# Performance work log

Measured on AMD Instinct MI355X. Metric: run time of the kernel, lower is better.

The kernel has to match this reference:

```python
import math
import jax, jax.numpy as jnp
import numpy as np

D_MODEL = 256
N_HEADS = 4
HEAD_DIM = D_MODEL // N_HEADS
MAX_REL = 30


def _rel_pos_encodings(t, d_model):
    # sinusoidal table over clipped relative distances -> [t, t, d_model]
    n = 2 * MAX_REL + 1
    positions = jnp.arange(n, dtype=jnp.float32)[:, None]
    div_term = jnp.exp(jnp.arange(0, d_model, 2, dtype=jnp.float32) * (-math.log(10000.0) / d_model))
    ang = positions * div_term                      # [n, d/2]
    enc = jnp.stack([jnp.sin(ang), jnp.cos(ang)], axis=-1).reshape(n, d_model)
    rng = jnp.arange(t)
    final_mat = jnp.clip(rng[None, :] - rng[:, None], -MAX_REL, MAX_REL) + MAX_REL  # [t, t]
    return enc[final_mat]                           # [t, t, d_model]


def setup_inputs() -> dict:
    key = jax.random.key(0)
    ks = jax.random.split(key, 12)
    d = D_MODEL
    s = 1.0 / math.sqrt(d)
    inp = {
        "inputs": jax.random.normal(ks[0], (16, 512, d), dtype=jnp.float32),
        "ln_gamma": jnp.ones((d,), jnp.float32),
        "ln_beta": jnp.zeros((d,), jnp.float32),
        "Wq": jax.random.normal(ks[1], (d, d), jnp.float32) * s,
        "bq": jnp.zeros((d,), jnp.float32),
        "Wk": jax.random.normal(ks[2], (d, d), jnp.float32) * s,
        "bk": jnp.zeros((d,), jnp.float32),
        "Wv": jax.random.normal(ks[3], (d, d), jnp.float32) * s,
        "bv": jnp.zeros((d,), jnp.float32),
        "Wpos": jax.random.normal(ks[4], (d, d), jnp.float32) * s,
        "bpos": jnp.zeros((d,), jnp.float32),
        "Wo": jax.random.normal(ks[5], (d, d), jnp.float32) * s,
        "bo": jnp.zeros((d,), jnp.float32),
        "u_bias": jax.random.normal(ks[6], (1, N_HEADS, 1, HEAD_DIM), jnp.float32) * 0.02,
        "v_bias": jax.random.normal(ks[7], (1, N_HEADS, 1, HEAD_DIM), jnp.float32) * 0.02,
    }
    return inp


def reference(inputs, ln_gamma, ln_beta, Wq, bq, Wk, bk, Wv, bv, Wpos, bpos, Wo, bo, u_bias, v_bias):
    b, t, d = inputs.shape
    h, hd = N_HEADS, HEAD_DIM
    # LayerNorm (eps=1e-5, torch default)
    mu = jnp.mean(inputs, axis=-1, keepdims=True)
    var = jnp.mean(jnp.square(inputs - mu), axis=-1, keepdims=True)
    x = (inputs - mu) * jax.lax.rsqrt(var + 1e-5) * ln_gamma + ln_beta

    def split_heads(y):
        return y.reshape(b, t, h, hd).transpose(0, 2, 1, 3)  # b h t d

    q = split_heads(x @ Wq.T + bq)
    k = split_heads(x @ Wk.T + bk)
    v = split_heads(x @ Wv.T + bv)

    rel = jax.lax.stop_gradient(_rel_pos_encodings(t, d))    # [t, t, d]
    pos = (rel @ Wpos.T + bpos).reshape(t, t, h, hd)         # [t1, t2, h, hd]

    qk_score = jnp.einsum('bhtd,bhsd->bhts', q + u_bias, k)
    pos_score = jnp.einsum('bhtd,tshd->bhts', q + v_bias, pos)
    scores = (qk_score + pos_score) / math.sqrt(hd)
    attn = jax.nn.softmax(scores, axis=-1)
    ctx = jnp.einsum('bhts,bhsd->bhtd', attn, v)
    ctx = ctx.transpose(0, 2, 1, 3).reshape(b, t, d)
    return ctx @ Wo.T + bo
```

## Files before the change

kernel.cpp:

```cpp
#include <hip/hip_runtime.h>
#include <hip/hip_bf16.h>
#include <math.h>

#define B 16
#define T 512
#define D 256
#define H 4
#define HD 64
#define MAXREL 30
#define NREL 61
#define M_ROWS (B*T)
#define QBLK 128

typedef __attribute__((ext_vector_type(8))) short bf16x8;
typedef __attribute__((ext_vector_type(4))) float f32x4;
typedef unsigned short ush;

__device__ inline ush f2b(float f) {
    __hip_bfloat16 h = __float2bfloat16(f);
    union { __hip_bfloat16 h; ush u; } c; c.h = h; return c.u;
}
__device__ inline float b2f(ush u) {
    union { ush u; __hip_bfloat16 h; } c; c.u = u; return __bfloat162float(c.h);
}
__device__ inline unsigned int pk2(float a, float b) {
    __hip_bfloat162 h = __float22bfloat162_rn(make_float2(a, b));
    union { __hip_bfloat162 h; unsigned int u; } c; c.h = h; return c.u;
}
__device__ inline int swz(int row, int byteoff) {
    return row * 128 + (byteoff ^ ((row & 7) << 4));
}
__device__ inline int swz256(int row, int byteoff) {
    return row * 256 + (byteoff ^ ((row & 7) << 4));
}
__device__ inline int swz512(int row, int byteoff) {
    return row * 512 + (byteoff ^ ((row & 7) << 4));
}

#define SCL 0.1803368801111204f

__global__ __launch_bounds__(256) void prep_kernel(const float* __restrict__ x,
                                                   const float* __restrict__ gamma,
                                                   const float* __restrict__ beta,
                                                   ush* __restrict__ xb,
                                                   const float* __restrict__ Wq, const float* __restrict__ Wk,
                                                   const float* __restrict__ Wv, const float* __restrict__ Wo,
                                                   ush* __restrict__ wb,
                                                   const float* __restrict__ Wpos,
                                                   const float* __restrict__ bpos,
                                                   ush* __restrict__ pospb) {
    __shared__ __attribute__((aligned(16))) ush wpS[64 * 256];
    int bid = blockIdx.x;
    int tid = threadIdx.x;
    if (bid < 512) {
        int lane = tid & 63;
        float4 g = *(const float4*)(gamma + lane * 4);
        float4 bb = *(const float4*)(beta + lane * 4);
        #pragma unroll
        for (int it = 0; it < 4; ++it) {
            int row = bid * 16 + it * 4 + (tid >> 6);
            const float* xr = x + (size_t)row * D;
            float4 v = *(const float4*)(xr + lane * 4);
            float s = v.x + v.y + v.z + v.w;
            #pragma unroll
            for (int off = 32; off; off >>= 1) s += __shfl_xor(s, off);
            float mu = s * (1.f / 256.f);
            float dx = v.x - mu, dy = v.y - mu, dz = v.z - mu, dw = v.w - mu;
            float vs = dx*dx + dy*dy + dz*dz + dw*dw;
            #pragma unroll
            for (int off = 32; off; off >>= 1) vs += __shfl_xor(vs, off);
            float rstd = rsqrtf(vs * (1.f / 256.f) + 1e-5f);
            ushort4 o;
            o.x = f2b(dx * rstd * g.x + bb.x);
            o.y = f2b(dy * rstd * g.y + bb.y);
            o.z = f2b(dz * rstd * g.z + bb.z);
            o.w = f2b(dw * rstd * g.w + bb.w);
            *(ushort4*)(xb + (size_t)row * D + lane * 4) = o;
        }
    } else if (bid < 512 + 256) {
        int b2 = bid - 512;
        int z = b2 >> 6, xblk = b2 & 63;
        const float* src = z == 0 ? Wq : z == 1 ? Wk : z == 2 ? Wv : Wo;
        int idx = (xblk * 256 + tid) * 4;
        float4 v = *(const float4*)(src + idx);
        ushort4 o;
        o.x = f2b(v.x); o.y = f2b(v.y); o.z = f2b(v.z); o.w = f2b(v.w);
        *(ushort4*)(wb + (size_t)z * 65536 + idx) = o;
    } else {
        int h = bid - 768;
        int w = tid >> 6, l = tid & 63, lg = l >> 4, ln = l & 15;
        const float* wsrc = Wpos + (size_t)(h * 64) * D;
        #pragma unroll
        for (int c = 0; c < 16; ++c) {
            int idx = c * 256 + tid;
            int row = idx >> 6, col = (idx & 63) * 4;
            float4 v = *(const float4*)(wsrc + (size_t)row * D + col);
            ushort4 o; o.x = f2b(v.x); o.y = f2b(v.y); o.z = f2b(v.z); o.w = f2b(v.w);
            *(ushort4*)((char*)wpS + swz512(row, col * 2)) = o;
        }
        int p = w * 16 + ln;
        bf16x8 af[8];
        #pragma unroll
        for (int ks = 0; ks < 8; ++ks) {
            #pragma unroll
            for (int j = 0; j < 8; ++j) {
                int k = ks * 32 + lg * 8 + j;
                int i = k >> 1;
                float dt = __expf(-(2.f * i) * (9.210340371976184f / 256.f));
                float ang = (float)p * dt;
                float v = (k & 1) ? __cosf(ang) : __sinf(ang);
                af[ks][j] = (short)f2b(v);
            }
        }
        __syncthreads();
        f32x4 acc[4] = {};
        #pragma unroll
        for (int ks = 0; ks < 8; ++ks) {
            int kbyte = (ks * 32 + lg * 8) * 2;
            #pragma unroll
            for (int ct = 0; ct < 4; ++ct) {
                bf16x8 bf = *(const bf16x8*)((const char*)wpS + swz512(ct * 16 + ln, kbyte));
                acc[ct] = __builtin_amdgcn_mfma_f32_16x16x32_bf16(af[ks], bf, acc[ct], 0, 0, 0);
            }
        }
        #pragma unroll
        for (int ct = 0; ct < 4; ++ct) {
            int dcol = ct * 16 + ln;
            float bb = bpos[h * 64 + dcol];
            #pragma unroll
            for (int r = 0; r < 4; ++r) {
                int pr = w * 16 + lg * 4 + r;
                pospb[(size_t)h * 4096 + pr * 64 + dcol] = f2b(acc[ct][r] + bb);
            }
        }
    }
}

__global__ __launch_bounds__(256, 3) void qkv_mfma(const ush* __restrict__ A,
                                                   const ush* __restrict__ wball,
                                                   const float* __restrict__ bq,
                                                   const float* __restrict__ bk,
                                                   const float* __restrict__ bv,
                                                   ush* __restrict__ qb,
                                                   ush* __restrict__ kbuf,
                                                   ush* __restrict__ vtb) {
    __shared__ __attribute__((aligned(16))) ush A_s[128 * 128];
    __shared__ __attribute__((aligned(16))) ush B_s[64 * 128];
    int tid = threadIdx.x;
    int w = tid >> 6, l = tid & 63;
    int lg = l >> 4, ln = l & 15;
    int wr = w >> 1, wc = w & 1;
    int i0 = blockIdx.x * 128;
    int j0 = blockIdx.y * 64;
    int z = blockIdx.z;
    const ush* Wp = wball + (size_t)z * 65536 + (size_t)j0 * D;
    const ush* Ap = A + (size_t)i0 * D;
    const float* bias = z == 0 ? bq : (z == 1 ? bk : bv);
    f32x4 acc[2][4] = {};

    #pragma unroll 1
    for (int kb2 = 0; kb2 < 2; ++kb2) {
        int k0 = kb2 * 128;
        if (kb2) __syncthreads();
        #pragma unroll
        for (int c = 0; c < 8; ++c) {
            int u = c * 256 + tid;
            int row = u >> 4, sub = u & 15;
            *(bf16x8*)((char*)A_s + swz256(row, sub * 16)) = *(const bf16x8*)(Ap + (size_t)row * D + k0 + sub * 8);
        }
        #pragma unroll
        for (int c = 0; c < 4; ++c) {
            int u = c * 256 + tid;
            int row = u >> 4, sub = u & 15;
            *(bf16x8*)((char*)B_s + swz256(row, sub * 16)) = *(const bf16x8*)(Wp + (size_t)row * D + k0 + sub * 8);
        }
        __syncthreads();
        __builtin_amdgcn_s_setprio(1);
        #pragma unroll
        for (int ksub = 0; ksub < 4; ++ksub) {
            int kbyte = ksub * 64 + lg * 16;
            bf16x8 af[2], bfr[4];
            #pragma unroll
            for (int mi = 0; mi < 2; ++mi)
                af[mi] = *(const bf16x8*)((const char*)B_s + swz256(wr * 32 + mi * 16 + ln, kbyte));
            #pragma unroll
            for (int ni = 0; ni < 4; ++ni)
                bfr[ni] = *(const bf16x8*)((const char*)A_s + swz256(wc * 64 + ni * 16 + ln, kbyte));
            #pragma unroll
            for (int mi = 0; mi < 2; ++mi)
                #pragma unroll
                for (int ni = 0; ni < 4; ++ni)
                    acc[mi][ni] = __builtin_amdgcn_mfma_f32_16x16x32_bf16(af[mi], bfr[ni], acc[mi][ni], 0, 0, 0);
        }
        __builtin_amdgcn_s_setprio(0);
    }

    if (z == 2) {
        #pragma unroll
        for (int mi = 0; mi < 2; ++mi) {
            int jb = j0 + wr * 32 + mi * 16 + lg * 4;
            float4 bv4 = *(const float4*)(bias + jb);
            float bvv[4] = {bv4.x, bv4.y, bv4.z, bv4.w};
            #pragma unroll
            for (int ni = 0; ni < 4; ++ni) {
                int t = i0 + wc * 64 + ni * 16 + ln;
                #pragma unroll
                for (int r = 0; r < 4; ++r)
                    vtb[(size_t)(jb + r) * M_ROWS + t] = f2b(acc[mi][ni][r] + bvv[r]);
            }
        }
    } else {
        ush* ob = (z == 0) ? qb : kbuf;
        #pragma unroll
        for (int mi = 0; mi < 2; ++mi) {
            int jb = j0 + wr * 32 + mi * 16 + lg * 4;
            float4 bv4 = *(const float4*)(bias + jb);
            #pragma unroll
            for (int ni = 0; ni < 4; ++ni) {
                int t = i0 + wc * 64 + ni * 16 + ln;
                ushort4 o;
                o.x = f2b(acc[mi][ni][0] + bv4.x); o.y = f2b(acc[mi][ni][1] + bv4.y);
                o.z = f2b(acc[mi][ni][2] + bv4.z); o.w = f2b(acc[mi][ni][3] + bv4.w);
                *(ushort4*)(ob + (size_t)t * D + jb) = o;
            }
        }
    }
}

__global__ __launch_bounds__(256, 2) void outproj_mfma(const ush* __restrict__ A,
                                                       const ush* __restrict__ W,
                                                       const float* __restrict__ bias,
                                                       float* __restrict__ of) {
    __shared__ __attribute__((aligned(16))) ush A_s[64 * 128];
    __shared__ __attribute__((aligned(16))) ush B_s[64 * 128];
    int tid = threadIdx.x;
    int w = tid >> 6, l = tid & 63;
    int lg = l >> 4, ln = l & 15;
    int wr = w >> 1, wc = w & 1;
    int i0 = blockIdx.x * 64;
    int j0 = blockIdx.y * 64;
    const ush* Ap = A + (size_t)i0 * D;
    const ush* Wp = W + (size_t)j0 * D;
    f32x4 acc[2][2] = {};

    #pragma unroll 1
    for (int kb2 = 0; kb2 < 2; ++kb2) {
        int k0 = kb2 * 128;
        if (kb2) __syncthreads();
        #pragma unroll
        for (int c = 0; c < 4; ++c) {
            int u = c * 256 + tid;
            int row = u >> 4, sub = u & 15;
            *(bf16x8*)((char*)A_s + swz256(row, sub * 16)) = *(const bf16x8*)(Ap + (size_t)row * D + k0 + sub * 8);
            *(bf16x8*)((char*)B_s + swz256(row, sub * 16)) = *(const bf16x8*)(Wp + (size_t)row * D + k0 + sub * 8);
        }
        __syncthreads();
        __builtin_amdgcn_s_setprio(1);
        #pragma unroll
        for (int ksub = 0; ksub < 4; ++ksub) {
            int kbyte = ksub * 64 + lg * 16;
            bf16x8 af[2], bfr[2];
            #pragma unroll
            for (int mi = 0; mi < 2; ++mi)
                af[mi] = *(const bf16x8*)((const char*)B_s + swz256(wr * 32 + mi * 16 + ln, kbyte));
            #pragma unroll
            for (int ni = 0; ni < 2; ++ni)
                bfr[ni] = *(const bf16x8*)((const char*)A_s + swz256(wc * 32 + ni * 16 + ln, kbyte));
            #pragma unroll
            for (int mi = 0; mi < 2; ++mi)
                #pragma unroll
                for (int ni = 0; ni < 2; ++ni)
                    acc[mi][ni] = __builtin_amdgcn_mfma_f32_16x16x32_bf16(af[mi], bfr[ni], acc[mi][ni], 0, 0, 0);
        }
        __builtin_amdgcn_s_setprio(0);
    }

    #pragma unroll
    for (int mi = 0; mi < 2; ++mi) {
        int jb = j0 + wr * 32 + mi * 16 + lg * 4;
        float4 bv4 = *(const float4*)(bias + jb);
        #pragma unroll
        for (int ni = 0; ni < 2; ++ni) {
            int t = i0 + wc * 32 + ni * 16 + ln;
            float4 o;
            o.x = acc[mi][ni][0] + bv4.x; o.y = acc[mi][ni][1] + bv4.y;
            o.z = acc[mi][ni][2] + bv4.z; o.w = acc[mi][ni][3] + bv4.w;
            *(float4*)(of + (size_t)t * D + jb) = o;
        }
    }
}

__global__ __launch_bounds__(512, 2) void attn_mfma(const ush* __restrict__ qb,
                                                    const ush* __restrict__ kb,
                                                    const ush* __restrict__ vtb,
                                                    const ush* __restrict__ pospb,
                                                    const float* __restrict__ u_bias,
                                                    const float* __restrict__ v_bias,
                                                    ush* __restrict__ ctxb) {
    __shared__ __attribute__((aligned(16))) ush Kd[2][64 * 64];
    __shared__ __attribute__((aligned(16))) ush Vd[2][64 * 64];
    __shared__ __attribute__((aligned(16))) ush pdS[8][16 * 66];
    __shared__ __attribute__((aligned(16))) ush PlS[8][16 * 64];

    int tid = threadIdx.x;
    int w = tid >> 6;
    int l = tid & 63;
    int lg = l >> 4, ln = l & 15;
    int bh = blockIdx.x;
    int b = bh >> 2, h = bh & 3;
    int t0 = blockIdx.y * QBLK;
    const size_t baseBH = ((size_t)b * T) * D + h * HD;

    bf16x8 qu[2], qv[2];
    {
        const ush* qrow = qb + baseBH + (size_t)(t0 + w * 16 + ln) * D;
        int c0 = lg * 8;
        #pragma unroll
        for (int ks = 0; ks < 2; ++ks) {
            bf16x8 ld = *(const bf16x8*)(qrow + ks * 32 + c0);
            float4 ub0 = *(const float4*)(u_bias + h * HD + ks * 32 + c0);
            float4 ub1 = *(const float4*)(u_bias + h * HD + ks * 32 + c0 + 4);
            float4 vb0 = *(const float4*)(v_bias + h * HD + ks * 32 + c0);
            float4 vb1 = *(const float4*)(v_bias + h * HD + ks * 32 + c0 + 4);
            float ubv[8] = {ub0.x,ub0.y,ub0.z,ub0.w,ub1.x,ub1.y,ub1.z,ub1.w};
            float vbv[8] = {vb0.x,vb0.y,vb0.z,vb0.w,vb1.x,vb1.y,vb1.z,vb1.w};
            #pragma unroll
            for (int j = 0; j < 8; ++j) {
                float f = b2f((ush)ld[j]);
                qu[ks][j] = (short)f2b((f + ubv[j]) * SCL);
                qv[ks][j] = (short)f2b((f + vbv[j]) * SCL);
            }
        }
    }

    int r0 = tid >> 3, c0 = tid & 7;
    const ush* kbase = kb + baseBH;
    const ush* vbase = vtb + (size_t)(h * HD) * M_ROWS + (size_t)b * T;
    const ush* pbase = pospb + (size_t)h * 4096;

    {
        bf16x8 pp0 = *(const bf16x8*)(pbase + r0 * 64 + c0 * 8);
        bf16x8 k0 = *(const bf16x8*)(kbase + (size_t)r0 * D + c0 * 8);
        bf16x8 v0 = *(const bf16x8*)(vbase + (size_t)r0 * M_ROWS + c0 * 8);
        *(bf16x8*)((char*)Kd[1] + swz(r0, c0 * 16)) = pp0;
        *(bf16x8*)((char*)Kd[0] + swz(r0, c0 * 16)) = k0;
        *(bf16x8*)((char*)Vd[0] + swz(r0, c0 * 16)) = v0;
    }
    bf16x8 sk0 = *(const bf16x8*)(kbase + (size_t)(64 + r0) * D + c0 * 8);
    bf16x8 sv0 = *(const bf16x8*)(vbase + (size_t)r0 * M_ROWS + 64 + c0 * 8);
    __syncthreads();

    ush* pdW = pdS[w];
    {
        f32x4 pacc[4] = {};
        #pragma unroll
        for (int ks = 0; ks < 2; ++ks)
            #pragma unroll
            for (int ct = 0; ct < 4; ++ct) {
                bf16x8 bf = *(const bf16x8*)((const char*)Kd[1] + swz(ct * 16 + ln, (ks * 32 + lg * 8) * 2));
                pacc[ct] = __builtin_amdgcn_mfma_f32_16x16x32_bf16(qv[ks], bf, pacc[ct], 0, 0, 0);
            }
        #pragma unroll
        for (int ct = 0; ct < 4; ++ct)
            #pragma unroll
            for (int r = 0; r < 4; ++r)
                pdW[(lg * 4 + r) * 66 + ct * 16 + ln] = f2b(pacc[ct][r]);
    }
    float pdlo = b2f(pdW[ln * 66 + 0]);
    float pdhi = b2f(pdW[ln * 66 + 60]);
    __syncthreads();

    f32x4 lacc = {};
    f32x4 o_acc[4] = {};
    ush* pw = PlS[w];
    bf16x8 ones;
    #pragma unroll
    for (int j = 0; j < 8; ++j) ones[j] = (short)0x3F80;
    int cur = 0;

    for (int st = 0; st < 8; ++st) {
        int s0 = st * 64;
        if (st < 7) {
            *(bf16x8*)((char*)Kd[cur ^ 1] + swz(r0, c0 * 16)) = sk0;
            *(bf16x8*)((char*)Vd[cur ^ 1] + swz(r0, c0 * 16)) = sv0;
        }
        if (st < 6) {
            int sn = s0 + 128;
            sk0 = *(const bf16x8*)(kbase + (size_t)(sn + r0) * D + c0 * 8);
            sv0 = *(const bf16x8*)(vbase + (size_t)r0 * M_ROWS + sn + c0 * 8);
        }

        const char* Kc = (const char*)Kd[cur];
        const char* Vc = (const char*)Vd[cur];

        int dlt = s0 - t0;
        float cinit;
        if (dlt >= 192) cinit = pdhi;
        else if (dlt <= -128) cinit = pdlo;
        else cinit = 0.f;
        f32x4 sacc[4];
        #pragma unroll
        for (int ct = 0; ct < 4; ++ct)
            #pragma unroll
            for (int r = 0; r < 4; ++r) sacc[ct][r] = cinit;

        __builtin_amdgcn_s_setprio(1);
        #pragma unroll
        for (int ks = 0; ks < 2; ++ks)
            #pragma unroll
            for (int ct = 0; ct < 4; ++ct) {
                bf16x8 kf = *(const bf16x8*)(Kc + swz(ct * 16 + ln, (ks * 32 + lg * 8) * 2));
                sacc[ct] = __builtin_amdgcn_mfma_f32_16x16x32_bf16(kf, qu[ks], sacc[ct], 0, 0, 0);
            }
        __builtin_amdgcn_s_setprio(0);

        if (dlt > -128 && dlt < 192) {
            int t_glob = t0 + w * 16 + ln;
            #pragma unroll
            for (int ct = 0; ct < 4; ++ct) {
                #pragma unroll
                for (int r = 0; r < 4; ++r) {
                    int s_g = s0 + ct * 16 + lg * 4 + r;
                    int rel = s_g - t_glob;
                    rel = rel < -MAXREL ? -MAXREL : (rel > MAXREL ? MAXREL : rel);
                    sacc[ct][r] += b2f(pdW[ln * 66 + rel + MAXREL]);
                }
            }
        }

        #pragma unroll
        for (int ct = 0; ct < 4; ++ct)
            #pragma unroll
            for (int r = 0; r < 4; ++r)
                sacc[ct][r] = exp2f(sacc[ct][r]);

        #pragma unroll
        for (int ct = 0; ct < 4; ++ct)
            #pragma unroll
            for (int rr = 0; rr < 2; ++rr)
                *(unsigned int*)((char*)pw + swz(ln, (ct * 16 + lg * 4 + rr * 2) * 2)) =
                    pk2(sacc[ct][rr * 2], sacc[ct][rr * 2 + 1]);

        __builtin_amdgcn_s_setprio(1);
        #pragma unroll
        for (int ks = 0; ks < 2; ++ks) {
            bf16x8 pa = *(const bf16x8*)((const char*)pw + swz(ln, (ks * 32 + lg * 8) * 2));
            #pragma unroll
            for (int cd = 0; cd < 4; ++cd) {
                bf16x8 bv8 = *(const bf16x8*)(Vc + swz(cd * 16 + ln, (ks * 32 + lg * 8) * 2));
                o_acc[cd] = __builtin_amdgcn_mfma_f32_16x16x32_bf16(pa, bv8, o_acc[cd], 0, 0, 0);
            }
            lacc = __builtin_amdgcn_mfma_f32_16x16x32_bf16(pa, ones, lacc, 0, 0, 0);
        }
        __builtin_amdgcn_s_setprio(0);

        __syncthreads();
        cur ^= 1;
    }

    float inv[4];
    #pragma unroll
    for (int r = 0; r < 4; ++r) inv[r] = 1.f / lacc[r];
    #pragma unroll
    for (int cd = 0; cd < 4; ++cd)
        #pragma unroll
        for (int r = 0; r < 4; ++r) {
            int t_loc = w * 16 + lg * 4 + r;
            ctxb[baseBH + (size_t)(t0 + t_loc) * D + cd * 16 + ln] = f2b(o_acc[cd][r] * inv[r]);
        }
}

extern "C" void kernel_launch(void* const* d_in, const int* in_sizes, int n_in,
                              void* d_out, int out_size, void* d_ws, size_t ws_size,
                              hipStream_t stream) {
    const float* inputs  = (const float*)d_in[0];
    const float* ln_g    = (const float*)d_in[1];
    const float* ln_b    = (const float*)d_in[2];
    const float* Wq      = (const float*)d_in[3];
    const float* bq      = (const float*)d_in[4];
    const float* Wk      = (const float*)d_in[5];
    const float* bk      = (const float*)d_in[6];
    const float* Wv      = (const float*)d_in[7];
    const float* bv      = (const float*)d_in[8];
    const float* Wpos    = (const float*)d_in[9];
    const float* bpos    = (const float*)d_in[10];
    const float* Wo      = (const float*)d_in[11];
    const float* bo      = (const float*)d_in[12];
    const float* u_bias  = (const float*)d_in[13];
    const float* v_bias  = (const float*)d_in[14];
    float* out = (float*)d_out;

    char* w = (char*)d_ws;
    ush* xb    = (ush*)w;  w += (size_t)M_ROWS * D * 2;
    ush* qb    = (ush*)w;  w += (size_t)M_ROWS * D * 2;
    ush* kbuf  = (ush*)w;  w += (size_t)M_ROWS * D * 2;
    ush* vtb   = (ush*)w;  w += (size_t)M_ROWS * D * 2;
    ush* ctxb  = (ush*)w;  w += (size_t)M_ROWS * D * 2;
    ush* wb    = (ush*)w;  w += (size_t)4 * 65536 * 2;
    ush* pospb = (ush*)w;  w += (size_t)4 * 64 * 64 * 2;

    prep_kernel<<<512 + 256 + 4, 256, 0, stream>>>(inputs, ln_g, ln_b, xb,
                                                   Wq, Wk, Wv, Wo, wb,
                                                   Wpos, bpos, pospb);

    qkv_mfma<<<dim3(M_ROWS / 128, 4, 3), 256, 0, stream>>>(xb, wb, bq, bk, bv, qb, kbuf, vtb);

    attn_mfma<<<dim3(B * H, T / QBLK), 512, 0, stream>>>(qb, kbuf, vtb, pospb, u_bias, v_bias, ctxb);

    outproj_mfma<<<dim3(M_ROWS / 64, 4), 256, 0, stream>>>(ctxb, wb + 3 * 65536, bo, out);
}
```

Before: 41.23 us.

## Split attention KV range across two blocks and merge partials in out-projection

Attention blocks now each process half of the key/value sequence, doubling grid size. Unnormalized fp32 partial outputs and row sums are written out, and the out-projection kernel sums the two halves, normalizes and converts to bf16 while staging its A tile. This aims to raise occupancy and CU utilization for the attention stage. The cost is extra fp32 intermediate traffic and per-element combine work in the projection load path. Launch bounds for attention are raised to allow more resident blocks.

```diff
diff --git a/kernel.cpp b/kernel.cpp
--- a/kernel.cpp
+++ b/kernel.cpp
@@ -227,7 +227,10 @@
     }
 }
 
-__global__ __launch_bounds__(256, 2) void outproj_mfma(const ush* __restrict__ A,
+__global__ __launch_bounds__(256, 2) void outproj_mfma(const float* __restrict__ op0,
+                                                       const float* __restrict__ op1,
+                                                       const float* __restrict__ lp0,
+                                                       const float* __restrict__ lp1,
                                                        const ush* __restrict__ W,
                                                        const float* __restrict__ bias,
                                                        float* __restrict__ of) {
@@ -239,7 +242,6 @@
     int wr = w >> 1, wc = w & 1;
     int i0 = blockIdx.x * 64;
     int j0 = blockIdx.y * 64;
-    const ush* Ap = A + (size_t)i0 * D;
     const ush* Wp = W + (size_t)j0 * D;
     f32x4 acc[2][2] = {};
 
@@ -251,7 +253,25 @@
         for (int c = 0; c < 4; ++c) {
             int u = c * 256 + tid;
             int row = u >> 4, sub = u & 15;
-            *(bf16x8*)((char*)A_s + swz256(row, sub * 16)) = *(const bf16x8*)(Ap + (size_t)row * D + k0 + sub * 8);
+            int trow = i0 + row;
+            int j = k0 + sub * 8;
+            int hh = j >> 6;
+            float lsum = lp0[trow * H + hh] + lp1[trow * H + hh];
+            float rl = 1.f / lsum;
+            const float* p0 = op0 + (size_t)trow * D + j;
+            const float* p1 = op1 + (size_t)trow * D + j;
+            float4 a0 = *(const float4*)p0, a1 = *(const float4*)(p0 + 4);
+            float4 b0 = *(const float4*)p1, b1 = *(const float4*)(p1 + 4);
+            bf16x8 o;
+            o[0] = (short)f2b((a0.x + b0.x) * rl);
+            o[1] = (short)f2b((a0.y + b0.y) * rl);
+            o[2] = (short)f2b((a0.z + b0.z) * rl);
+            o[3] = (short)f2b((a0.w + b0.w) * rl);
+            o[4] = (short)f2b((a1.x + b1.x) * rl);
+            o[5] = (short)f2b((a1.y + b1.y) * rl);
+            o[6] = (short)f2b((a1.z + b1.z) * rl);
+            o[7] = (short)f2b((a1.w + b1.w) * rl);
+            *(bf16x8*)((char*)A_s + swz256(row, sub * 16)) = o;
             *(bf16x8*)((char*)B_s + swz256(row, sub * 16)) = *(const bf16x8*)(Wp + (size_t)row * D + k0 + sub * 8);
         }
         __syncthreads();
@@ -290,13 +310,14 @@
     }
 }
 
-__global__ __launch_bounds__(512, 2) void attn_mfma(const ush* __restrict__ qb,
+__global__ __launch_bounds__(512, 4) void attn_mfma(const ush* __restrict__ qb,
                                                     const ush* __restrict__ kb,
                                                     const ush* __restrict__ vtb,
                                                     const ush* __restrict__ pospb,
                                                     const float* __restrict__ u_bias,
                                                     const float* __restrict__ v_bias,
-                                                    ush* __restrict__ ctxb) {
+                                                    float* __restrict__ opart,
+                                                    float* __restrict__ lpart) {
     __shared__ __attribute__((aligned(16))) ush Kd[2][64 * 64];
     __shared__ __attribute__((aligned(16))) ush Vd[2][64 * 64];
     __shared__ __attribute__((aligned(16))) ush pdS[8][16 * 66];
@@ -309,6 +330,8 @@
     int bh = blockIdx.x;
     int b = bh >> 2, h = bh & 3;
     int t0 = blockIdx.y * QBLK;
+    int half = blockIdx.z;
+    int sbase = half * 256;
     const size_t baseBH = ((size_t)b * T) * D + h * HD;
 
     bf16x8 qu[2], qv[2];
@@ -340,14 +363,14 @@
 
     {
         bf16x8 pp0 = *(const bf16x8*)(pbase + r0 * 64 + c0 * 8);
-        bf16x8 k0 = *(const bf16x8*)(kbase + (size_t)r0 * D + c0 * 8);
-        bf16x8 v0 = *(const bf16x8*)(vbase + (size_t)r0 * M_ROWS + c0 * 8);
+        bf16x8 k0 = *(const bf16x8*)(kbase + (size_t)(sbase + r0) * D + c0 * 8);
+        bf16x8 v0 = *(const bf16x8*)(vbase + (size_t)r0 * M_ROWS + sbase + c0 * 8);
         *(bf16x8*)((char*)Kd[1] + swz(r0, c0 * 16)) = pp0;
         *(bf16x8*)((char*)Kd[0] + swz(r0, c0 * 16)) = k0;
         *(bf16x8*)((char*)Vd[0] + swz(r0, c0 * 16)) = v0;
     }
-    bf16x8 sk0 = *(const bf16x8*)(kbase + (size_t)(64 + r0) * D + c0 * 8);
-    bf16x8 sv0 = *(const bf16x8*)(vbase + (size_t)r0 * M_ROWS + 64 + c0 * 8);
+    bf16x8 sk0 = *(const bf16x8*)(kbase + (size_t)(sbase + 64 + r0) * D + c0 * 8);
+    bf16x8 sv0 = *(const bf16x8*)(vbase + (size_t)r0 * M_ROWS + sbase + 64 + c0 * 8);
     __syncthreads();
 
     ush* pdW = pdS[w];
@@ -378,13 +401,13 @@
     for (int j = 0; j < 8; ++j) ones[j] = (short)0x3F80;
     int cur = 0;
 
-    for (int st = 0; st < 8; ++st) {
-        int s0 = st * 64;
-        if (st < 7) {
+    for (int st = 0; st < 4; ++st) {
+        int s0 = sbase + st * 64;
+        if (st < 3) {
             *(bf16x8*)((char*)Kd[cur ^ 1] + swz(r0, c0 * 16)) = sk0;
             *(bf16x8*)((char*)Vd[cur ^ 1] + swz(r0, c0 * 16)) = sv0;
         }
-        if (st < 6) {
+        if (st < 2) {
             int sn = s0 + 128;
             sk0 = *(const bf16x8*)(kbase + (size_t)(sn + r0) * D + c0 * 8);
             sv0 = *(const bf16x8*)(vbase + (size_t)r0 * M_ROWS + sn + c0 * 8);
@@ -458,16 +481,22 @@
         cur ^= 1;
     }
 
-    float inv[4];
-    #pragma unroll
-    for (int r = 0; r < 4; ++r) inv[r] = 1.f / lacc[r];
+    float* od = opart + (size_t)half * M_ROWS * D;
     #pragma unroll
     for (int cd = 0; cd < 4; ++cd)
         #pragma unroll
         for (int r = 0; r < 4; ++r) {
             int t_loc = w * 16 + lg * 4 + r;
-            ctxb[baseBH + (size_t)(t0 + t_loc) * D + cd * 16 + ln] = f2b(o_acc[cd][r] * inv[r]);
-        }
+            od[(size_t)(b * T + t0 + t_loc) * D + h * HD + cd * 16 + ln] = o_acc[cd][r];
+        }
+    if (ln == 0) {
+        float* ld = lpart + (size_t)half * M_ROWS * H;
+        #pragma unroll
+        for (int r = 0; r < 4; ++r) {
+            int t_loc = w * 16 + lg * 4 + r;
+            ld[(size_t)(b * T + t0 + t_loc) * H + h] = lacc[r];
+        }
+    }
 }
 
 extern "C" void kernel_launch(void* const* d_in, const int* in_sizes, int n_in,
@@ -495,9 +524,10 @@
     ush* qb    = (ush*)w;  w += (size_t)M_ROWS * D * 2;
     ush* kbuf  = (ush*)w;  w += (size_t)M_ROWS * D * 2;
     ush* vtb   = (ush*)w;  w += (size_t)M_ROWS * D * 2;
-    ush* ctxb  = (ush*)w;  w += (size_t)M_ROWS * D * 2;
     ush* wb    = (ush*)w;  w += (size_t)4 * 65536 * 2;
     ush* pospb = (ush*)w;  w += (size_t)4 * 64 * 64 * 2;
+    float* opart = (float*)w; w += (size_t)2 * M_ROWS * D * 4;
+    float* lpart = (float*)w; w += (size_t)2 * M_ROWS * H * 4;
 
     prep_kernel<<<512 + 256 + 4, 256, 0, stream>>>(inputs, ln_g, ln_b, xb,
                                                    Wq, Wk, Wv, Wo, wb,
@@ -505,7 +535,10 @@
 
     qkv_mfma<<<dim3(M_ROWS / 128, 4, 3), 256, 0, stream>>>(xb, wb, bq, bk, bv, qb, kbuf, vtb);
 
-    attn_mfma<<<dim3(B * H, T / QBLK), 512, 0, stream>>>(qb, kbuf, vtb, pospb, u_bias, v_bias, ctxb);
-
-    outproj_mfma<<<dim3(M_ROWS / 64, 4), 256, 0, stream>>>(ctxb, wb + 3 * 65536, bo, out);
-}
+    attn_mfma<<<dim3(B * H, T / QBLK, 2), 512, 0, stream>>>(qb, kbuf, vtb, pospb, u_bias, v_bias,
+                                                            opart, lpart);
+
+    outproj_mfma<<<dim3(M_ROWS / 64, 4), 256, 0, stream>>>(opart, opart + (size_t)M_ROWS * D,
+                                                           lpart, lpart + (size_t)M_ROWS * H,
+                                                           wb + 3 * 65536, bo, out);
+}
```

Result: slower. 46.13 us (+11.9%).
